# Kernel tuning notes

Hardware: AMD Instinct MI355X
Metric: run time of the kernel (lower is better)

The kernel has to match this reference:

```python
import jax, jax.numpy as jnp
import numpy as np

B, N, D, H = 256, 40, 256, 256      # molecules, atoms/molecule, pc_hidden, pred_hidden
nS, nC, nB = 40, 5, 5               # n_SYMBOLS, n_FORMAL_CHARGES, n_BOND_TYPES
NEG_SLOPE = 0.01                    # F.leaky_relu default


def _lrelu(x):
    return jnp.where(x >= 0, x, NEG_SLOPE * x)


def setup_inputs() -> dict:
    key = jax.random.key(0)
    ks = jax.random.split(key, 7)
    def w(k, shape, fan_in):
        return jax.random.normal(k, shape, jnp.float32) / np.float32(np.sqrt(fan_in))
    return {
        "yhat": jax.random.normal(ks[0], (B, N, D), jnp.float32),
        "Ws1": w(ks[1], (D, H), D),      "bs1": jnp.zeros((H,), jnp.float32),
        "Ws2": w(ks[2], (H, nS), H),     "bs2": jnp.zeros((nS,), jnp.float32),
        "Wc1": w(ks[3], (D, H), D),      "bc1": jnp.zeros((H,), jnp.float32),
        "Wc2": w(ks[4], (H, nC), H),     "bc2": jnp.zeros((nC,), jnp.float32),
        "Wb1": w(ks[5], (2 * D, H), 2 * D), "bb1": jnp.zeros((H,), jnp.float32),
        "Wb2": w(ks[6], (H, nB), H),     "bb2": jnp.zeros((nB,), jnp.float32),
    }


def reference(yhat, Ws1, bs1, Ws2, bs2, Wc1, bc1, Wc2, bc2, Wb1, bb1, Wb2, bb2):
    # Per-atom symbol / charge heads (2-layer MLP with leaky_relu)
    symbols = _lrelu(yhat @ Ws1 + bs1) @ Ws2 + bs2          # [B, N, nS]
    charges = _lrelu(yhat @ Wc1 + bc1) @ Wc2 + bc2          # [B, N, nC]

    # Pairwise bond head: concat(x_i, x_j) @ Wb1 == x_i @ Wb1[:D] + x_j @ Wb1[D:]
    # (avoids materializing the [B, N, N, 2D] concat tensor)
    p1 = yhat @ Wb1[:D]                                      # [B, N, H]
    p2 = yhat @ Wb1[D:]                                      # [B, N, H]
    h = _lrelu(p1[:, :, None, :] + p2[:, None, :, :] + bb1)  # [B, N, N, H]
    bonds = h @ Wb2 + bb2                                    # [B, N, N, nB]
    bonds = bonds + jnp.swapaxes(bonds, 1, 2)                # symmetrize (i,j)+(j,i)

    return (symbols.reshape(-1, nS),
            charges.reshape(-1, nC),
            bonds.reshape(-1, nB))
```

## Files before the change

kernel.cpp:

```cpp
#include <hip/hip_runtime.h>
#include <hip/hip_bf16.h>

typedef unsigned short u16;
typedef __attribute__((ext_vector_type(4))) int   int4v;
typedef __attribute__((ext_vector_type(4))) unsigned int uint4v;
typedef __attribute__((ext_vector_type(4))) unsigned short ushort4v;
typedef __attribute__((ext_vector_type(4))) float floatx4;
typedef __attribute__((ext_vector_type(8))) short bf16x8;

#define LRELU_NS 0.01f
#define SK 264

__device__ __forceinline__ float bitsToF(unsigned int b) {
    union { unsigned int u; float f; } v; v.u = b << 16; return v.f;
}
__device__ __forceinline__ float bfLo(unsigned int d) {
    union { unsigned int u; float f; } v; v.u = d << 16; return v.f;
}
__device__ __forceinline__ float bfHi(unsigned int d) {
    union { unsigned int u; float f; } v; v.u = d & 0xffff0000u; return v.f;
}
__device__ __forceinline__ u16 f2bf(float f) {
    __hip_bfloat16 h = __float2bfloat16(f);
    return *reinterpret_cast<u16*>(&h);
}
__device__ __forceinline__ float lrelu(float v) {
    return fmaxf(v, LRELU_NS * v);
}
__device__ __forceinline__ u16 ldW(const void* p, int i, int isF32) {
    return isF32 ? f2bf(((const float*)p)[i]) : ((const u16*)p)[i];
}
__device__ __forceinline__ float ldF(const void* p, int i, int isF32) {
    return isF32 ? ((const float*)p)[i]
                 : bitsToF((unsigned int)((const u16*)p)[i]);
}

__device__ __forceinline__ int computeIsF32(const u16* y, int* cnt, int t) {
    if (t == 0) *cnt = 0;
    __syncthreads();
    if (t < 256) {
        u16 v = y[2 * t];
        int e = (v >> 7) & 0xFF;
        if (v == 0 || (e >= 96 && e < 160)) atomicAdd(cnt, 1);
    }
    __syncthreads();
    return (*cnt < 192) ? 1 : 0;
}

__global__ __launch_bounds__(256) void pack_kernel(
    const void* __restrict__ yhat,
    const void* __restrict__ Ws1, const void* __restrict__ Wc1,
    const void* __restrict__ Wb1, const void* __restrict__ Ws2,
    const void* __restrict__ Wc2,
    const void* __restrict__ bs1, const void* __restrict__ bc1,
    const void* __restrict__ bb1, const void* __restrict__ bs2,
    const void* __restrict__ bc2, const void* __restrict__ bb2,
    u16* __restrict__ WallT, u16* __restrict__ W2T, float* __restrict__ biasF)
{
    __shared__ int fcnt;
    const int bid = blockIdx.x, t = threadIdx.x;
    const int isF32 = computeIsF32((const u16*)yhat, &fcnt, t);
    if (bid < 64) {
        __shared__ u16 tile[64][65];
        const int c0 = (bid & 15) * 64;
        const int k0 = (bid >> 4) * 64;
        const void* src; int coff; int roff = 0;
        if (c0 < 256)      { src = Ws1; coff = c0; }
        else if (c0 < 512) { src = Wc1; coff = c0 - 256; }
        else if (c0 < 768) { src = Wb1; coff = c0 - 512; }
        else               { src = Wb1; coff = c0 - 768; roff = 256; }
        const int cc = t & 63, kk0 = t >> 6;
        #pragma unroll
        for (int i = 0; i < 16; ++i) {
            int kk = kk0 + i * 4;
            tile[kk][cc] = ldW(src, (k0 + kk + roff) * 256 + coff + cc, isF32);
        }
        __syncthreads();
        const int kk2 = t & 63, cc0 = t >> 6;
        #pragma unroll
        for (int i = 0; i < 16; ++i) {
            int cc2 = cc0 + i * 4;
            WallT[(c0 + cc2) * 256 + (k0 + kk2)] = tile[kk2][cc2];
        }
    } else if (bid < 128) {
        int e2 = (bid - 64) * 256 + t;
        int c = e2 >> 8, k = e2 & 255;
        u16 v = 0;
        if (c < 40)                 v = ldW(Ws2, k * 40 + c, isF32);
        else if (c >= 48 && c < 53) v = ldW(Wc2, k * 5 + (c - 48), isF32);
        W2T[c * 256 + k] = v;
    } else {
        int idx = (bid - 128) * 256 + t;
        float v = 0.f;
        if (idx < 256)       v = ldF(bs1, idx, isF32);
        else if (idx < 512)  v = ldF(bc1, idx - 256, isF32);
        else if (idx < 768)  v = ldF(bb1, idx - 512, isF32);
        else if (idx < 808)  v = ldF(bs2, idx - 768, isF32);
        else if (idx < 813)  v = ldF(bc2, idx - 808, isF32);
        else if (idx >= 816 && idx < 821) v = ldF(bb2, idx - 816, isF32);
        biasF[idx] = v;
    }
}

__global__ __launch_bounds__(256) void heads_kernel(
    const void* __restrict__ Xv, const u16* __restrict__ WallT,
    const u16* __restrict__ W2T, const float* __restrict__ biasF,
    void* __restrict__ outv)
{
    __shared__ u16 Xs[64 * SK];
    __shared__ u16 Hb[64 * SK];
    __shared__ int fcnt;
    const int t = threadIdx.x;
    const int bm0 = blockIdx.x * 64;
    const int head = blockIdx.y;
    const int isF32 = computeIsF32((const u16*)Xv, &fcnt, t);

    if (isF32) {
        const floatx4* __restrict__ src = (const floatx4*)((const float*)Xv + bm0 * 256);
        #pragma unroll
        for (int it = 0; it < 16; ++it) {
            int cid = t + it * 256;
            int row = cid >> 6, ch = cid & 63;
            floatx4 f = src[cid];
            ushort4v u;
            u[0] = f2bf(f[0]); u[1] = f2bf(f[1]); u[2] = f2bf(f[2]); u[3] = f2bf(f[3]);
            *(ushort4v*)&Xs[row * SK + ch * 4] = u;
        }
    } else {
        const int4v* __restrict__ src = (const int4v*)((const u16*)Xv + bm0 * 256);
        #pragma unroll
        for (int it = 0; it < 8; ++it) {
            int cid = t + it * 256;
            int row = cid >> 5, ch = cid & 31;
            *(int4v*)&Xs[row * SK + ch * 8] = src[cid];
        }
    }
    __syncthreads();

    const int w = t >> 6, l = t & 63;
    const int ml = l & 15, kq = l >> 4, r0 = kq * 4;

    for (int n = 0; n < 4; ++n) {
        const int ct = w + 4 * n;
        floatx4 acc[4] = {};
        #pragma unroll
        for (int ks = 0; ks < 8; ++ks) {
            const int k0 = ks * 32 + kq * 8;
            bf16x8 bf = *(const bf16x8*)&WallT[(head * 256 + ct * 16 + ml) * 256 + k0];
            #pragma unroll
            for (int mt = 0; mt < 4; ++mt) {
                bf16x8 a = *(const bf16x8*)&Xs[(mt * 16 + ml) * SK + k0];
                acc[mt] = __builtin_amdgcn_mfma_f32_16x16x32_bf16(a, bf, acc[mt], 0, 0, 0);
            }
        }
        const int col = ct * 16 + ml;
        const float bias = biasF[head * 256 + col];
        #pragma unroll
        for (int mt = 0; mt < 4; ++mt)
            #pragma unroll
            for (int r = 0; r < 4; ++r)
                Hb[(mt * 16 + r0 + r) * SK + col] = f2bf(lrelu(acc[mt][r] + bias));
    }
    __syncthreads();

    const int nct = (head == 0) ? 3 : 1;
    const int c0  = (head == 0) ? 0 : 48;
    floatx4 acc2[3] = {};
    #pragma unroll
    for (int ks = 0; ks < 8; ++ks) {
        const int k0 = ks * 32 + kq * 8;
        bf16x8 a = *(const bf16x8*)&Hb[(w * 16 + ml) * SK + k0];
        #pragma unroll
        for (int j = 0; j < 3; ++j) {
            if (j < nct) {
                bf16x8 bf = *(const bf16x8*)&W2T[(c0 + j * 16 + ml) * 256 + k0];
                acc2[j] = __builtin_amdgcn_mfma_f32_16x16x32_bf16(a, bf, acc2[j], 0, 0, 0);
            }
        }
    }
    #pragma unroll
    for (int j = 0; j < 3; ++j) {
        if (j < nct) {
            const int col = j * 16 + ml;
            const int lim = (head == 0) ? 40 : 5;
            if (col < lim) {
                const float bias = biasF[(head == 0 ? 768 : 808) + col];
                #pragma unroll
                for (int r = 0; r < 4; ++r) {
                    const int row = bm0 + w * 16 + r0 + r;
                    const int o = (head == 0) ? row * 40 + col
                                              : 409600 + row * 5 + col;
                    const float v = acc2[j][r] + bias;
                    if (isF32) ((float*)outv)[o] = v;
                    else ((__hip_bfloat16*)outv)[o] = __float2bfloat16(v);
                }
            }
        }
    }
}

__global__ __launch_bounds__(512) void l1p_kernel(
    const void* __restrict__ Xv, const u16* __restrict__ WallT,
    const float* __restrict__ biasF,
    u16* __restrict__ P1g, u16* __restrict__ P2g)
{
    __shared__ u16 Xs[64 * SK];
    __shared__ int fcnt;
    const int t = threadIdx.x;
    const int bm0 = blockIdx.x * 64;
    const int isF32 = computeIsF32((const u16*)Xv, &fcnt, t);

    if (isF32) {
        const floatx4* __restrict__ src = (const floatx4*)((const float*)Xv + bm0 * 256);
        #pragma unroll
        for (int s = 0; s < 8; ++s) {
            int cid = t + s * 512;
            int row = cid >> 6, ch = cid & 63;
            floatx4 f = src[cid];
            ushort4v u;
            u[0] = f2bf(f[0]); u[1] = f2bf(f[1]); u[2] = f2bf(f[2]); u[3] = f2bf(f[3]);
            *(ushort4v*)&Xs[row * SK + ch * 4] = u;
        }
    } else {
        const int4v* __restrict__ src = (const int4v*)((const u16*)Xv + bm0 * 256);
        #pragma unroll
        for (int s = 0; s < 4; ++s) {
            int cid = t + s * 512;
            int row = cid >> 5, ch = cid & 31;
            *(int4v*)&Xs[row * SK + ch * 8] = src[cid];
        }
    }
    __syncthreads();

    const int w = t >> 6, l = t & 63;
    const int ml = l & 15, kq = l >> 4, r0 = kq * 4;
    const int ct = blockIdx.y * 8 + w;
    const int gc = ct * 16 + ml;

    floatx4 acc[4] = {};
    #pragma unroll
    for (int ks = 0; ks < 8; ++ks) {
        const int k0 = ks * 32 + kq * 8;
        bf16x8 bf = *(const bf16x8*)&WallT[(512 + gc) * 256 + k0];
        #pragma unroll
        for (int mt = 0; mt < 4; ++mt) {
            bf16x8 a = *(const bf16x8*)&Xs[(mt * 16 + ml) * SK + k0];
            acc[mt] = __builtin_amdgcn_mfma_f32_16x16x32_bf16(a, bf, acc[mt], 0, 0, 0);
        }
    }
    const float bias = (gc < 256) ? biasF[512 + gc] : 0.f;
    u16* __restrict__ dst = (gc < 256) ? P1g : P2g;
    const int col = gc & 255;
    #pragma unroll
    for (int mt = 0; mt < 4; ++mt)
        #pragma unroll
        for (int r = 0; r < 4; ++r)
            dst[(bm0 + mt * 16 + r0 + r) * 256 + col] = f2bf(acc[mt][r] + bias);
}

__global__ __launch_bounds__(512, 4) void pairf_kernel(
    const void* __restrict__ Xv,
    const u16* __restrict__ P1g, const u16* __restrict__ P2g,
    const void* __restrict__ Wb2, const float* __restrict__ biasF,
    void* __restrict__ outv)
{
    __shared__ u16 Pq[4][16 * SK];
    __shared__ u16 WsB[16 * 264];
    __shared__ int fcnt;
    const int t = threadIdx.x, mol = blockIdx.x;
    const int y = blockIdx.y;
    const int it = (y < 3) ? 0 : (y < 5) ? 1 : 2;
    const int jt = (y < 3) ? y : (y < 5) ? (y - 2) : 2;
    const int isF32 = computeIsF32((const u16*)Xv, &fcnt, t);

    #pragma unroll
    for (int s = 0; s < 4; ++s) {
        const int cid = t + s * 512;
        const int buf = cid >> 9, r = (cid >> 5) & 15, ch = cid & 31;
        const int tile = (buf < 2) ? it : jt;
        const u16* __restrict__ src = (buf & 1) ? P2g : P1g;
        const int arow = tile * 16 + r;
        int4v v = {0, 0, 0, 0};
        if (arow < 40) v = *(const int4v*)&src[(mol * 40 + arow) * 256 + ch * 8];
        *(int4v*)&Pq[buf][r * SK + ch * 8] = v;
    }
    #pragma unroll
    for (int s = 0; s < 8; ++s) {
        const int e2 = t + s * 512;
        const int c = e2 >> 8, k = e2 & 255;
        WsB[c * 264 + k] = (c < 5) ? ldW(Wb2, k * 5 + c, isF32) : (u16)0;
    }
    __syncthreads();

    const int w = t >> 6, l = t & 63;
    const int ml = l & 15, kq = l >> 4, r0 = kq * 4;

    bf16x8 wf[8];
    #pragma unroll
    for (int ks = 0; ks < 8; ++ks)
        wf[ks] = *(const bf16x8*)&WsB[ml * 264 + ks * 32 + kq * 8];
    const float b2x2 = 2.f * biasF[816 + ml];

    for (int ii = 0; ii < 2; ++ii) {
        const int iloc = w + 8 * ii;
        const int i = it * 16 + iloc;
        if (i >= 40) continue;
        floatx4 acc = {};
        #pragma unroll
        for (int ks = 0; ks < 8; ++ks) {
            const int k0 = ks * 32 + kq * 8;
            uint4v a1 = *(const uint4v*)&Pq[0][iloc * SK + k0];
            uint4v a2 = *(const uint4v*)&Pq[1][iloc * SK + k0];
            uint4v b1 = *(const uint4v*)&Pq[2][ml * SK + k0];
            uint4v b2 = *(const uint4v*)&Pq[3][ml * SK + k0];
            bf16x8 af;
            #pragma unroll
            for (int d = 0; d < 4; ++d) {
                const float sLo = lrelu(bfLo(a1[d]) + bfLo(b2[d]))
                                + lrelu(bfLo(b1[d]) + bfLo(a2[d]));
                const float sHi = lrelu(bfHi(a1[d]) + bfHi(b2[d]))
                                + lrelu(bfHi(b1[d]) + bfHi(a2[d]));
                af[2 * d]     = (short)f2bf(sLo);
                af[2 * d + 1] = (short)f2bf(sHi);
            }
            acc = __builtin_amdgcn_mfma_f32_16x16x32_bf16(af, wf[ks], acc, 0, 0, 0);
        }
        if (ml < 5) {
            #pragma unroll
            for (int r = 0; r < 4; ++r) {
                const int j = jt * 16 + r0 + r;
                if (j < 40 && (it != jt || j >= i)) {
                    const float v = acc[r] + b2x2;
                    const int o1 = 460800 + (mol * 1600 + i * 40 + j) * 5 + ml;
                    if (isF32) ((float*)outv)[o1] = v;
                    else ((__hip_bfloat16*)outv)[o1] = __float2bfloat16(v);
                    if (it != jt || j > i) {
                        const int o2 = 460800 + (mol * 1600 + j * 40 + i) * 5 + ml;
                        if (isF32) ((float*)outv)[o2] = v;
                        else ((__hip_bfloat16*)outv)[o2] = __float2bfloat16(v);
                    }
                }
            }
        }
    }
}

__global__ __launch_bounds__(512) void bonds_kernel(
    const void* __restrict__ Xv, const u16* __restrict__ WallT,
    const void* __restrict__ Wb2, const float* __restrict__ biasF,
    void* __restrict__ outv)
{
    __shared__ u16 Xm[48 * SK];
    __shared__ u16 P1L[48 * SK];
    __shared__ u16 P2L[48 * SK];
    __shared__ u16 WsB[16 * 264];
    __shared__ float fbuf[8000];
    __shared__ int fcnt;
    const int t = threadIdx.x, b = blockIdx.x;
    const int isF32 = computeIsF32((const u16*)Xv, &fcnt, t);

    if (isF32) {
        const floatx4* __restrict__ src = (const floatx4*)((const float*)Xv + b * 10240);
        #pragma unroll
        for (int it = 0; it < 5; ++it) {
            int cid = t + it * 512;
            int row = cid >> 6, ch = cid & 63;
            floatx4 f = src[cid];
            ushort4v u;
            u[0] = f2bf(f[0]); u[1] = f2bf(f[1]); u[2] = f2bf(f[2]); u[3] = f2bf(f[3]);
            *(ushort4v*)&Xm[row * SK + ch * 4] = u;
        }
        {
            int row = 40 + (t >> 6), ch = t & 63;
            ushort4v z = {0, 0, 0, 0};
            *(ushort4v*)&Xm[row * SK + ch * 4] = z;
        }
    } else {
        const int4v* __restrict__ src = (const int4v*)((const u16*)Xv + b * 10240);
        #pragma unroll
        for (int it = 0; it < 3; ++it) {
            int cid = t + it * 512;
            int row = cid >> 5, ch = cid & 31;
            if (cid < 1280) *(int4v*)&Xm[row * SK + ch * 8] = src[cid];
            else { int4v z = {0, 0, 0, 0}; *(int4v*)&Xm[row * SK + ch * 8] = z; }
        }
    }
    #pragma unroll
    for (int it = 0; it < 8; ++it) {
        int e2 = t + it * 512;
        int c = e2 >> 8, k = e2 & 255;
        WsB[c * 264 + k] = (c < 5) ? ldW(Wb2, k * 5 + c, isF32) : (u16)0;
    }
    __syncthreads();

    const int w = t >> 6, l = t & 63;
    const int ml = l & 15, kq = l >> 4, r0 = kq * 4;

    for (int n = 0; n < 4; ++n) {
        const int gc = (w + 8 * n) * 16 + ml;
        floatx4 acc[3] = {};
        #pragma unroll
        for (int ks = 0; ks < 8; ++ks) {
            const int k0 = ks * 32 + kq * 8;
            bf16x8 bf = *(const bf16x8*)&WallT[(512 + gc) * 256 + k0];
            #pragma unroll
            for (int i = 0; i < 3; ++i) {
                bf16x8 a = *(const bf16x8*)&Xm[(i * 16 + ml) * SK + k0];
                acc[i] = __builtin_amdgcn_mfma_f32_16x16x32_bf16(a, bf, acc[i], 0, 0, 0);
            }
        }
        u16* dst = (gc < 256) ? P1L : P2L;
        const int col = gc & 255;
        const float bias = (gc < 256) ? biasF[512 + gc] : 0.f;
        #pragma unroll
        for (int i = 0; i < 3; ++i)
            #pragma unroll
            for (int r = 0; r < 4; ++r)
                dst[(i * 16 + r0 + r) * SK + col] = f2bf(acc[i][r] + bias);
    }
    __syncthreads();

    bf16x8 wf[8];
    #pragma unroll
    for (int ks = 0; ks < 8; ++ks)
        wf[ks] = *(const bf16x8*)&WsB[ml * 264 + ks * 32 + kq * 8];

    for (int m = 0; m < 5; ++m) {
        const int i = w + 8 * m;
        uint4v pa8[8];
        #pragma unroll
        for (int ks = 0; ks < 8; ++ks)
            pa8[ks] = *(const uint4v*)&P1L[i * SK + ks * 32 + kq * 8];
        for (int jt = 0; jt < 3; ++jt) {
            floatx4 acc = {};
            #pragma unroll
            for (int ks = 0; ks < 8; ++ks) {
                const int k0 = ks * 32 + kq * 8;
                uint4v pa = pa8[ks];
                uint4v pb = *(const uint4v*)&P2L[(jt * 16 + ml) * SK + k0];
                bf16x8 af;
                #pragma unroll
                for (int d = 0; d < 4; ++d) {
                    af[2 * d]     = (short)f2bf(lrelu(bfLo(pa[d]) + bfLo(pb[d])));
                    af[2 * d + 1] = (short)f2bf(lrelu(bfHi(pa[d]) + bfHi(pb[d])));
                }
                acc = __builtin_amdgcn_mfma_f32_16x16x32_bf16(af, wf[ks], acc, 0, 0, 0);
            }
            if (ml < 5) {
                #pragma unroll
                for (int r = 0; r < 4; ++r) {
                    const int j = jt * 16 + r0 + r;
                    if (j < 40) fbuf[(i * 40 + j) * 5 + ml] = acc[r];
                }
            }
        }
    }
    __syncthreads();

    const int base = 460800 + b * 8000;
    for (int e = t; e < 8000; e += 512) {
        int pr = e / 5, c = e - pr * 5;
        int i = pr / 40, j = pr - (pr / 40) * 40;
        float v = fbuf[e] + fbuf[(j * 40 + i) * 5 + c] + 2.f * biasF[816 + c];
        if (isF32) ((float*)outv)[base + e] = v;
        else ((__hip_bfloat16*)outv)[base + e] = __float2bfloat16(v);
    }
}

extern "C" void kernel_launch(void* const* d_in, const int* in_sizes, int n_in,
                              void* d_out, int out_size, void* d_ws, size_t ws_size,
                              hipStream_t stream)
{
    const void* yhat = d_in[0];
    const void* Ws1  = d_in[1];
    const void* bs1  = d_in[2];
    const void* Ws2  = d_in[3];
    const void* bs2  = d_in[4];
    const void* Wc1  = d_in[5];
    const void* bc1  = d_in[6];
    const void* Wc2  = d_in[7];
    const void* bc2  = d_in[8];
    const void* Wb1  = d_in[9];
    const void* bb1  = d_in[10];
    const void* Wb2  = d_in[11];
    const void* bb2  = d_in[12];

    char* wsb = (char*)d_ws;
    float* biasF = (float*)(wsb + 4096);
    u16*   W2T   = (u16*)(wsb + 8192);
    u16*   WallT = (u16*)(wsb + 40960);
    const size_t P_OFF   = 565248;
    const size_t P_BYTES = (size_t)10240 * 256 * 2;
    const bool big = ws_size >= P_OFF + 2 * P_BYTES;

    pack_kernel<<<132, 256, 0, stream>>>(yhat, Ws1, Wc1, Wb1, Ws2, Wc2,
                                         bs1, bc1, bb1, bs2, bc2, bb2,
                                         WallT, W2T, biasF);
    heads_kernel<<<dim3(160, 2), 256, 0, stream>>>(yhat, WallT, W2T, biasF, d_out);
    if (big) {
        u16* P1g = (u16*)(wsb + P_OFF);
        u16* P2g = (u16*)(wsb + P_OFF + P_BYTES);
        l1p_kernel<<<dim3(160, 4), 512, 0, stream>>>(yhat, WallT, biasF, P1g, P2g);
        pairf_kernel<<<dim3(256, 6), 512, 0, stream>>>(yhat, P1g, P2g, Wb2, biasF, d_out);
    } else {
        bonds_kernel<<<256, 512, 0, stream>>>(yhat, WallT, Wb2, biasF, d_out);
    }
}
```

Measured before the change: 146.5 us.

## Merge all layer-1 GEMMs into one kernel and pair two rows per warp in pairf

All four first-layer projections (symbol hidden, charge hidden, P1, P2) now come from one kernel that loads X once per 64-row tile and writes the hidden activations to workspace. A small second-layer kernel then reads those hiddens back. This replaces the separate heads and l1p kernels, which each reloaded and converted X. In pairf each warp now processes its two i rows in one k-loop, sharing the b1/b2 shared-memory loads and interleaving two MFMA chains. The cost is an extra global round trip for the symbol and charge hidden activations, and the path needs a larger workspace, falling back to the old kernels otherwise.

```diff
diff --git a/kernel.cpp b/kernel.cpp
--- a/kernel.cpp
+++ b/kernel.cpp
@@ -102,12 +102,78 @@
     }
 }
 
-__global__ __launch_bounds__(256) void heads_kernel(
+__global__ __launch_bounds__(512) void l1all_kernel(
     const void* __restrict__ Xv, const u16* __restrict__ WallT,
-    const u16* __restrict__ W2T, const float* __restrict__ biasF,
-    void* __restrict__ outv)
+    const float* __restrict__ biasF,
+    u16* __restrict__ Hs, u16* __restrict__ Hc,
+    u16* __restrict__ P1g, u16* __restrict__ P2g)
 {
     __shared__ u16 Xs[64 * SK];
+    __shared__ int fcnt;
+    const int t = threadIdx.x;
+    const int bm0 = blockIdx.x * 64;
+    const int y = blockIdx.y;
+    const int isF32 = computeIsF32((const u16*)Xv, &fcnt, t);
+
+    if (isF32) {
+        const floatx4* __restrict__ src = (const floatx4*)((const float*)Xv + bm0 * 256);
+        #pragma unroll
+        for (int s = 0; s < 8; ++s) {
+            int cid = t + s * 512;
+            int row = cid >> 6, ch = cid & 63;
+            floatx4 f = src[cid];
+            ushort4v u;
+            u[0] = f2bf(f[0]); u[1] = f2bf(f[1]); u[2] = f2bf(f[2]); u[3] = f2bf(f[3]);
+            *(ushort4v*)&Xs[row * SK + ch * 4] = u;
+        }
+    } else {
+        const int4v* __restrict__ src = (const int4v*)((const u16*)Xv + bm0 * 256);
+        #pragma unroll
+        for (int s = 0; s < 4; ++s) {
+            int cid = t + s * 512;
+            int row = cid >> 5, ch = cid & 31;
+            *(int4v*)&Xs[row * SK + ch * 8] = src[cid];
+        }
+    }
+    __syncthreads();
+
+    const int w = t >> 6, l = t & 63;
+    const int ml = l & 15, kq = l >> 4, r0 = kq * 4;
+    u16* __restrict__ dstBase = (y == 0) ? Hs : (y == 1) ? Hc : (y == 2) ? P1g : P2g;
+
+    #pragma unroll
+    for (int n = 0; n < 2; ++n) {
+        const int ct = w + 8 * n;
+        const int col = ct * 16 + ml;
+        const int gc = y * 256 + col;
+        floatx4 acc[4] = {};
+        #pragma unroll
+        for (int ks = 0; ks < 8; ++ks) {
+            const int k0 = ks * 32 + kq * 8;
+            bf16x8 bf = *(const bf16x8*)&WallT[gc * 256 + k0];
+            #pragma unroll
+            for (int mt = 0; mt < 4; ++mt) {
+                bf16x8 a = *(const bf16x8*)&Xs[(mt * 16 + ml) * SK + k0];
+                acc[mt] = __builtin_amdgcn_mfma_f32_16x16x32_bf16(a, bf, acc[mt], 0, 0, 0);
+            }
+        }
+        const float bias = (y < 3) ? biasF[y * 256 + col] : 0.f;
+        #pragma unroll
+        for (int mt = 0; mt < 4; ++mt)
+            #pragma unroll
+            for (int r = 0; r < 4; ++r) {
+                float v = acc[mt][r] + bias;
+                if (y < 2) v = lrelu(v);
+                dstBase[(bm0 + mt * 16 + r0 + r) * 256 + col] = f2bf(v);
+            }
+    }
+}
+
+__global__ __launch_bounds__(256) void l2heads_kernel(
+    const void* __restrict__ Xv, const u16* __restrict__ Hs,
+    const u16* __restrict__ Hc, const u16* __restrict__ W2T,
+    const float* __restrict__ biasF, void* __restrict__ outv)
+{
     __shared__ u16 Hb[64 * SK];
     __shared__ int fcnt;
     const int t = threadIdx.x;
@@ -115,53 +181,18 @@
     const int head = blockIdx.y;
     const int isF32 = computeIsF32((const u16*)Xv, &fcnt, t);
 
-    if (isF32) {
-        const floatx4* __restrict__ src = (const floatx4*)((const float*)Xv + bm0 * 256);
-        #pragma unroll
-        for (int it = 0; it < 16; ++it) {
-            int cid = t + it * 256;
-            int row = cid >> 6, ch = cid & 63;
-            floatx4 f = src[cid];
-            ushort4v u;
-            u[0] = f2bf(f[0]); u[1] = f2bf(f[1]); u[2] = f2bf(f[2]); u[3] = f2bf(f[3]);
-            *(ushort4v*)&Xs[row * SK + ch * 4] = u;
-        }
-    } else {
-        const int4v* __restrict__ src = (const int4v*)((const u16*)Xv + bm0 * 256);
-        #pragma unroll
-        for (int it = 0; it < 8; ++it) {
-            int cid = t + it * 256;
-            int row = cid >> 5, ch = cid & 31;
-            *(int4v*)&Xs[row * SK + ch * 8] = src[cid];
-        }
+    const u16* __restrict__ Hg = (head == 0) ? Hs : Hc;
+    const int4v* __restrict__ src = (const int4v*)(Hg + bm0 * 256);
+    #pragma unroll
+    for (int it = 0; it < 8; ++it) {
+        int cid = t + it * 256;
+        int row = cid >> 5, ch = cid & 31;
+        *(int4v*)&Hb[row * SK + ch * 8] = src[cid];
     }
     __syncthreads();
 
     const int w = t >> 6, l = t & 63;
     const int ml = l & 15, kq = l >> 4, r0 = kq * 4;
-
-    for (int n = 0; n < 4; ++n) {
-        const int ct = w + 4 * n;
-        floatx4 acc[4] = {};
-        #pragma unroll
-        for (int ks = 0; ks < 8; ++ks) {
-            const int k0 = ks * 32 + kq * 8;
-            bf16x8 bf = *(const bf16x8*)&WallT[(head * 256 + ct * 16 + ml) * 256 + k0];
-            #pragma unroll
-            for (int mt = 0; mt < 4; ++mt) {
-                bf16x8 a = *(const bf16x8*)&Xs[(mt * 16 + ml) * SK + k0];
-                acc[mt] = __builtin_amdgcn_mfma_f32_16x16x32_bf16(a, bf, acc[mt], 0, 0, 0);
-            }
-        }
-        const int col = ct * 16 + ml;
-        const float bias = biasF[head * 256 + col];
-        #pragma unroll
-        for (int mt = 0; mt < 4; ++mt)
-            #pragma unroll
-            for (int r = 0; r < 4; ++r)
-                Hb[(mt * 16 + r0 + r) * SK + col] = f2bf(lrelu(acc[mt][r] + bias));
-    }
-    __syncthreads();
 
     const int nct = (head == 0) ? 3 : 1;
     const int c0  = (head == 0) ? 0 : 48;
@@ -199,65 +230,6 @@
     }
 }
 
-__global__ __launch_bounds__(512) void l1p_kernel(
-    const void* __restrict__ Xv, const u16* __restrict__ WallT,
-    const float* __restrict__ biasF,
-    u16* __restrict__ P1g, u16* __restrict__ P2g)
-{
-    __shared__ u16 Xs[64 * SK];
-    __shared__ int fcnt;
-    const int t = threadIdx.x;
-    const int bm0 = blockIdx.x * 64;
-    const int isF32 = computeIsF32((const u16*)Xv, &fcnt, t);
-
-    if (isF32) {
-        const floatx4* __restrict__ src = (const floatx4*)((const float*)Xv + bm0 * 256);
-        #pragma unroll
-        for (int s = 0; s < 8; ++s) {
-            int cid = t + s * 512;
-            int row = cid >> 6, ch = cid & 63;
-            floatx4 f = src[cid];
-            ushort4v u;
-            u[0] = f2bf(f[0]); u[1] = f2bf(f[1]); u[2] = f2bf(f[2]); u[3] = f2bf(f[3]);
-            *(ushort4v*)&Xs[row * SK + ch * 4] = u;
-        }
-    } else {
-        const int4v* __restrict__ src = (const int4v*)((const u16*)Xv + bm0 * 256);
-        #pragma unroll
-        for (int s = 0; s < 4; ++s) {
-            int cid = t + s * 512;
-            int row = cid >> 5, ch = cid & 31;
-            *(int4v*)&Xs[row * SK + ch * 8] = src[cid];
-        }
-    }
-    __syncthreads();
-
-    const int w = t >> 6, l = t & 63;
-    const int ml = l & 15, kq = l >> 4, r0 = kq * 4;
-    const int ct = blockIdx.y * 8 + w;
-    const int gc = ct * 16 + ml;
-
-    floatx4 acc[4] = {};
-    #pragma unroll
-    for (int ks = 0; ks < 8; ++ks) {
-        const int k0 = ks * 32 + kq * 8;
-        bf16x8 bf = *(const bf16x8*)&WallT[(512 + gc) * 256 + k0];
-        #pragma unroll
-        for (int mt = 0; mt < 4; ++mt) {
-            bf16x8 a = *(const bf16x8*)&Xs[(mt * 16 + ml) * SK + k0];
-            acc[mt] = __builtin_amdgcn_mfma_f32_16x16x32_bf16(a, bf, acc[mt], 0, 0, 0);
-        }
-    }
-    const float bias = (gc < 256) ? biasF[512 + gc] : 0.f;
-    u16* __restrict__ dst = (gc < 256) ? P1g : P2g;
-    const int col = gc & 255;
-    #pragma unroll
-    for (int mt = 0; mt < 4; ++mt)
-        #pragma unroll
-        for (int r = 0; r < 4; ++r)
-            dst[(bm0 + mt * 16 + r0 + r) * 256 + col] = f2bf(acc[mt][r] + bias);
-}
-
 __global__ __launch_bounds__(512, 4) void pairf_kernel(
     const void* __restrict__ Xv,
     const u16* __restrict__ P1g, const u16* __restrict__ P2g,
@@ -301,18 +273,18 @@
         wf[ks] = *(const bf16x8*)&WsB[ml * 264 + ks * 32 + kq * 8];
     const float b2x2 = 2.f * biasF[816 + ml];
 
-    for (int ii = 0; ii < 2; ++ii) {
-        const int iloc = w + 8 * ii;
-        const int i = it * 16 + iloc;
-        if (i >= 40) continue;
-        floatx4 acc = {};
-        #pragma unroll
-        for (int ks = 0; ks < 8; ++ks) {
-            const int k0 = ks * 32 + kq * 8;
-            uint4v a1 = *(const uint4v*)&Pq[0][iloc * SK + k0];
-            uint4v a2 = *(const uint4v*)&Pq[1][iloc * SK + k0];
-            uint4v b1 = *(const uint4v*)&Pq[2][ml * SK + k0];
-            uint4v b2 = *(const uint4v*)&Pq[3][ml * SK + k0];
+    const int i0 = it * 16 + w;
+    const int i1 = i0 + 8;
+    const bool do1 = (it != 2);
+    floatx4 acc0 = {}, acc1 = {};
+    #pragma unroll
+    for (int ks = 0; ks < 8; ++ks) {
+        const int k0 = ks * 32 + kq * 8;
+        const uint4v b1 = *(const uint4v*)&Pq[2][ml * SK + k0];
+        const uint4v b2 = *(const uint4v*)&Pq[3][ml * SK + k0];
+        {
+            const uint4v a1 = *(const uint4v*)&Pq[0][w * SK + k0];
+            const uint4v a2 = *(const uint4v*)&Pq[1][w * SK + k0];
             bf16x8 af;
             #pragma unroll
             for (int d = 0; d < 4; ++d) {
@@ -323,19 +295,52 @@
                 af[2 * d]     = (short)f2bf(sLo);
                 af[2 * d + 1] = (short)f2bf(sHi);
             }
-            acc = __builtin_amdgcn_mfma_f32_16x16x32_bf16(af, wf[ks], acc, 0, 0, 0);
-        }
-        if (ml < 5) {
+            acc0 = __builtin_amdgcn_mfma_f32_16x16x32_bf16(af, wf[ks], acc0, 0, 0, 0);
+        }
+        if (do1) {
+            const uint4v a1 = *(const uint4v*)&Pq[0][(w + 8) * SK + k0];
+            const uint4v a2 = *(const uint4v*)&Pq[1][(w + 8) * SK + k0];
+            bf16x8 af;
+            #pragma unroll
+            for (int d = 0; d < 4; ++d) {
+                const float sLo = lrelu(bfLo(a1[d]) + bfLo(b2[d]))
+                                + lrelu(bfLo(b1[d]) + bfLo(a2[d]));
+                const float sHi = lrelu(bfHi(a1[d]) + bfHi(b2[d]))
+                                + lrelu(bfHi(b1[d]) + bfHi(a2[d]));
+                af[2 * d]     = (short)f2bf(sLo);
+                af[2 * d + 1] = (short)f2bf(sHi);
+            }
+            acc1 = __builtin_amdgcn_mfma_f32_16x16x32_bf16(af, wf[ks], acc1, 0, 0, 0);
+        }
+    }
+
+    if (ml < 5) {
+        #pragma unroll
+        for (int r = 0; r < 4; ++r) {
+            const int j = jt * 16 + r0 + r;
+            if (j < 40 && (it != jt || j >= i0)) {
+                const float v = acc0[r] + b2x2;
+                const int o1 = 460800 + (mol * 1600 + i0 * 40 + j) * 5 + ml;
+                if (isF32) ((float*)outv)[o1] = v;
+                else ((__hip_bfloat16*)outv)[o1] = __float2bfloat16(v);
+                if (it != jt || j > i0) {
+                    const int o2 = 460800 + (mol * 1600 + j * 40 + i0) * 5 + ml;
+                    if (isF32) ((float*)outv)[o2] = v;
+                    else ((__hip_bfloat16*)outv)[o2] = __float2bfloat16(v);
+                }
+            }
+        }
+        if (do1) {
             #pragma unroll
             for (int r = 0; r < 4; ++r) {
                 const int j = jt * 16 + r0 + r;
-                if (j < 40 && (it != jt || j >= i)) {
-                    const float v = acc[r] + b2x2;
-                    const int o1 = 460800 + (mol * 1600 + i * 40 + j) * 5 + ml;
+                if (j < 40 && (it != jt || j >= i1)) {
+                    const float v = acc1[r] + b2x2;
+                    const int o1 = 460800 + (mol * 1600 + i1 * 40 + j) * 5 + ml;
                     if (isF32) ((float*)outv)[o1] = v;
                     else ((__hip_bfloat16*)outv)[o1] = __float2bfloat16(v);
-                    if (it != jt || j > i) {
-                        const int o2 = 460800 + (mol * 1600 + j * 40 + i) * 5 + ml;
+                    if (it != jt || j > i1) {
+                        const int o2 = 460800 + (mol * 1600 + j * 40 + i1) * 5 + ml;
                         if (isF32) ((float*)outv)[o2] = v;
                         else ((__hip_bfloat16*)outv)[o2] = __float2bfloat16(v);
                     }
@@ -343,6 +348,162 @@
             }
         }
     }
+}
+
+__global__ __launch_bounds__(256) void heads_kernel(
+    const void* __restrict__ Xv, const u16* __restrict__ WallT,
+    const u16* __restrict__ W2T, const float* __restrict__ biasF,
+    void* __restrict__ outv)
+{
+    __shared__ u16 Xs[64 * SK];
+    __shared__ u16 Hb[64 * SK];
+    __shared__ int fcnt;
+    const int t = threadIdx.x;
+    const int bm0 = blockIdx.x * 64;
+    const int head = blockIdx.y;
+    const int isF32 = computeIsF32((const u16*)Xv, &fcnt, t);
+
+    if (isF32) {
+        const floatx4* __restrict__ src = (const floatx4*)((const float*)Xv + bm0 * 256);
+        #pragma unroll
+        for (int it = 0; it < 16; ++it) {
+            int cid = t + it * 256;
+            int row = cid >> 6, ch = cid & 63;
+            floatx4 f = src[cid];
+            ushort4v u;
+            u[0] = f2bf(f[0]); u[1] = f2bf(f[1]); u[2] = f2bf(f[2]); u[3] = f2bf(f[3]);
+            *(ushort4v*)&Xs[row * SK + ch * 4] = u;
+        }
+    } else {
+        const int4v* __restrict__ src = (const int4v*)((const u16*)Xv + bm0 * 256);
+        #pragma unroll
+        for (int it = 0; it < 8; ++it) {
+            int cid = t + it * 256;
+            int row = cid >> 5, ch = cid & 31;
+            *(int4v*)&Xs[row * SK + ch * 8] = src[cid];
+        }
+    }
+    __syncthreads();
+
+    const int w = t >> 6, l = t & 63;
+    const int ml = l & 15, kq = l >> 4, r0 = kq * 4;
+
+    for (int n = 0; n < 4; ++n) {
+        const int ct = w + 4 * n;
+        floatx4 acc[4] = {};
+        #pragma unroll
+        for (int ks = 0; ks < 8; ++ks) {
+            const int k0 = ks * 32 + kq * 8;
+            bf16x8 bf = *(const bf16x8*)&WallT[(head * 256 + ct * 16 + ml) * 256 + k0];
+            #pragma unroll
+            for (int mt = 0; mt < 4; ++mt) {
+                bf16x8 a = *(const bf16x8*)&Xs[(mt * 16 + ml) * SK + k0];
+                acc[mt] = __builtin_amdgcn_mfma_f32_16x16x32_bf16(a, bf, acc[mt], 0, 0, 0);
+            }
+        }
+        const int col = ct * 16 + ml;
+        const float bias = biasF[head * 256 + col];
+        #pragma unroll
+        for (int mt = 0; mt < 4; ++mt)
+            #pragma unroll
+            for (int r = 0; r < 4; ++r)
+                Hb[(mt * 16 + r0 + r) * SK + col] = f2bf(lrelu(acc[mt][r] + bias));
+    }
+    __syncthreads();
+
+    const int nct = (head == 0) ? 3 : 1;
+    const int c0  = (head == 0) ? 0 : 48;
+    floatx4 acc2[3] = {};
+    #pragma unroll
+    for (int ks = 0; ks < 8; ++ks) {
+        const int k0 = ks * 32 + kq * 8;
+        bf16x8 a = *(const bf16x8*)&Hb[(w * 16 + ml) * SK + k0];
+        #pragma unroll
+        for (int j = 0; j < 3; ++j) {
+            if (j < nct) {
+                bf16x8 bf = *(const bf16x8*)&W2T[(c0 + j * 16 + ml) * 256 + k0];
+                acc2[j] = __builtin_amdgcn_mfma_f32_16x16x32_bf16(a, bf, acc2[j], 0, 0, 0);
+            }
+        }
+    }
+    #pragma unroll
+    for (int j = 0; j < 3; ++j) {
+        if (j < nct) {
+            const int col = j * 16 + ml;
+            const int lim = (head == 0) ? 40 : 5;
+            if (col < lim) {
+                const float bias = biasF[(head == 0 ? 768 : 808) + col];
+                #pragma unroll
+                for (int r = 0; r < 4; ++r) {
+                    const int row = bm0 + w * 16 + r0 + r;
+                    const int o = (head == 0) ? row * 40 + col
+                                              : 409600 + row * 5 + col;
+                    const float v = acc2[j][r] + bias;
+                    if (isF32) ((float*)outv)[o] = v;
+                    else ((__hip_bfloat16*)outv)[o] = __float2bfloat16(v);
+                }
+            }
+        }
+    }
+}
+
+__global__ __launch_bounds__(512) void l1p_kernel(
+    const void* __restrict__ Xv, const u16* __restrict__ WallT,
+    const float* __restrict__ biasF,
+    u16* __restrict__ P1g, u16* __restrict__ P2g)
+{
+    __shared__ u16 Xs[64 * SK];
+    __shared__ int fcnt;
+    const int t = threadIdx.x;
+    const int bm0 = blockIdx.x * 64;
+    const int isF32 = computeIsF32((const u16*)Xv, &fcnt, t);
+
+    if (isF32) {
+        const floatx4* __restrict__ src = (const floatx4*)((const float*)Xv + bm0 * 256);
+        #pragma unroll
+        for (int s = 0; s < 8; ++s) {
+            int cid = t + s * 512;
+            int row = cid >> 6, ch = cid & 63;
+            floatx4 f = src[cid];
+            ushort4v u;
+            u[0] = f2bf(f[0]); u[1] = f2bf(f[1]); u[2] = f2bf(f[2]); u[3] = f2bf(f[3]);
+            *(ushort4v*)&Xs[row * SK + ch * 4] = u;
+        }
+    } else {
+        const int4v* __restrict__ src = (const int4v*)((const u16*)Xv + bm0 * 256);
+        #pragma unroll
+        for (int s = 0; s < 4; ++s) {
+            int cid = t + s * 512;
+            int row = cid >> 5, ch = cid & 31;
+            *(int4v*)&Xs[row * SK + ch * 8] = src[cid];
+        }
+    }
+    __syncthreads();
+
+    const int w = t >> 6, l = t & 63;
+    const int ml = l & 15, kq = l >> 4, r0 = kq * 4;
+    const int ct = blockIdx.y * 8 + w;
+    const int gc = ct * 16 + ml;
+
+    floatx4 acc[4] = {};
+    #pragma unroll
+    for (int ks = 0; ks < 8; ++ks) {
+        const int k0 = ks * 32 + kq * 8;
+        bf16x8 bf = *(const bf16x8*)&WallT[(512 + gc) * 256 + k0];
+        #pragma unroll
+        for (int mt = 0; mt < 4; ++mt) {
+            bf16x8 a = *(const bf16x8*)&Xs[(mt * 16 + ml) * SK + k0];
+            acc[mt] = __builtin_amdgcn_mfma_f32_16x16x32_bf16(a, bf, acc[mt], 0, 0, 0);
+        }
+    }
+    const float bias = (gc < 256) ? biasF[512 + gc] : 0.f;
+    u16* __restrict__ dst = (gc < 256) ? P1g : P2g;
+    const int col = gc & 255;
+    #pragma unroll
+    for (int mt = 0; mt < 4; ++mt)
+        #pragma unroll
+        for (int r = 0; r < 4; ++r)
+            dst[(bm0 + mt * 16 + r0 + r) * 256 + col] = f2bf(acc[mt][r] + bias);
 }
 
 __global__ __launch_bounds__(512) void bonds_kernel(
@@ -489,20 +650,31 @@
     float* biasF = (float*)(wsb + 4096);
     u16*   W2T   = (u16*)(wsb + 8192);
     u16*   WallT = (u16*)(wsb + 40960);
-    const size_t P_OFF   = 565248;
     const size_t P_BYTES = (size_t)10240 * 256 * 2;
-    const bool big = ws_size >= P_OFF + 2 * P_BYTES;
+    u16* P1g = (u16*)(wsb + 565248);
+    u16* P2g = (u16*)(wsb + 565248 + P_BYTES);
+    u16* Hs  = (u16*)(wsb + 565248 + 2 * P_BYTES);
+    u16* Hc  = (u16*)(wsb + 565248 + 3 * P_BYTES);
+    const bool big  = ws_size >= 565248 + 2 * P_BYTES;
+    const bool bigH = ws_size >= 565248 + 4 * P_BYTES;
 
     pack_kernel<<<132, 256, 0, stream>>>(yhat, Ws1, Wc1, Wb1, Ws2, Wc2,
                                          bs1, bc1, bb1, bs2, bc2, bb2,
                                          WallT, W2T, biasF);
-    heads_kernel<<<dim3(160, 2), 256, 0, stream>>>(yhat, WallT, W2T, biasF, d_out);
-    if (big) {
-        u16* P1g = (u16*)(wsb + P_OFF);
-        u16* P2g = (u16*)(wsb + P_OFF + P_BYTES);
+    if (bigH) {
+        l1all_kernel<<<dim3(160, 4), 512, 0, stream>>>(yhat, WallT, biasF,
+                                                       Hs, Hc, P1g, P2g);
+        l2heads_kernel<<<dim3(160, 2), 256, 0, stream>>>(yhat, Hs, Hc, W2T,
+                                                         biasF, d_out);
+        pairf_kernel<<<dim3(256, 6), 512, 0, stream>>>(yhat, P1g, P2g, Wb2,
+                                                       biasF, d_out);
+    } else if (big) {
+        heads_kernel<<<dim3(160, 2), 256, 0, stream>>>(yhat, WallT, W2T, biasF, d_out);
         l1p_kernel<<<dim3(160, 4), 512, 0, stream>>>(yhat, WallT, biasF, P1g, P2g);
-        pairf_kernel<<<dim3(256, 6), 512, 0, stream>>>(yhat, P1g, P2g, Wb2, biasF, d_out);
+        pairf_kernel<<<dim3(256, 6), 512, 0, stream>>>(yhat, P1g, P2g, Wb2,
+                                                       biasF, d_out);
     } else {
+        heads_kernel<<<dim3(160, 2), 256, 0, stream>>>(yhat, WallT, W2T, biasF, d_out);
         bonds_kernel<<<256, 512, 0, stream>>>(yhat, WallT, Wb2, biasF, d_out);
     }
 }
```

New measurement: 149.1 us. About the same (+1.7%).
